# Optimization experiments

Hardware: AMD Instinct MI355X
Metric: run time of the kernel (lower is better)

Reference implementation:

```python
import jax, jax.numpy as jnp
import numpy as np

BLOCK_SIZE = 32
FP6_E2M3_MAX = 7.5

def _build_fp6_e2m3_grid():
    vals = set()
    for bits in range(64):
        s = (bits >> 5) & 1
        e = (bits >> 3) & 3
        m = bits & 7
        v = (m / 8.0) if e == 0 else (1.0 + m / 8.0) * 2.0 ** (e - 1)
        vals.add(-v if s else v)
    return np.array(sorted(vals), dtype=np.float32)

_GRID = jnp.asarray(_build_fp6_e2m3_grid())  # sorted 1-D fp32 grid (46 unique values)

def _nearest_on_grid(x, grid):
    # round-to-nearest on a sorted grid via searchsorted (matches torch reference)
    idx = jnp.clip(jnp.searchsorted(grid, x), 0, grid.shape[0] - 1)
    idx_lo = jnp.maximum(idx - 1, 0)
    v_hi = grid[idx]
    v_lo = grid[idx_lo]
    return jnp.where(jnp.abs(x - v_lo) <= jnp.abs(x - v_hi), v_lo, v_hi)

def _mx_quantize(t, eps=1e-30):
    # t: (rows, K) fp32, K divisible by BLOCK_SIZE
    rows, K = t.shape
    blocks = t.reshape(rows, K // BLOCK_SIZE, BLOCK_SIZE)
    scales = jnp.maximum(jnp.max(jnp.abs(blocks), axis=-1) / FP6_E2M3_MAX, eps)  # (rows, nb)
    q = _nearest_on_grid(blocks / scales[..., None], _GRID)  # fp6-simulated fp32
    return q, scales

def setup_inputs() -> dict:
    key = jax.random.key(0)
    k1, k2, k3 = jax.random.split(key, 3)
    x = jax.random.normal(k1, (8, 8192, 1024), dtype=jnp.float32)
    weight = jax.random.normal(k2, (1024, 1024), dtype=jnp.float32) * 0.02
    bias = jax.random.normal(k3, (1024,), dtype=jnp.float32) * 0.02
    return {"x": x, "weight": weight, "bias": bias}

def reference(x, weight, bias):
    batch_shape = x.shape[:-1]
    in_features = x.shape[-1]
    x2 = x.astype(jnp.float32).reshape(-1, in_features)      # (N, K)
    w2 = weight.astype(jnp.float32)                           # (J, K)
    xq, xs = _mx_quantize(x2)                                 # (N, nb, bs), (N, nb)
    wq, ws = _mx_quantize(w2)                                 # (J, nb, bs), (J, nb)
    # out[n, j] = sum_b xs[n,b] * ws[j,b] * dot(xq[n,b,:], wq[j,b,:])
    # == dequant(x) @ dequant(w).T  (fold fp32 scales into quantized blocks)
    xd = (xq * xs[..., None]).reshape(x2.shape)
    wd = (wq * ws[..., None]).reshape(w2.shape)
    out = xd @ wd.T + bias
    return out.reshape(*batch_shape, -1)
```

## Files before the change

kernel.cpp:

```cpp
#include <hip/hip_runtime.h>
#include <stdint.h>

#define K_DIM 1024
#define N_DIM 1024
#define M_DIM 65536

typedef __bf16 bf16_t;
typedef __bf16 bf16x8 __attribute__((ext_vector_type(8)));
typedef float f32x4 __attribute__((ext_vector_type(4)));

#define GLOAD_LDS16(g, l) __builtin_amdgcn_global_load_lds( \
    (const __attribute__((address_space(1))) void*)(g),     \
    (__attribute__((address_space(3))) void*)(l), 16, 0, 0)

#define VMCNT(n) asm volatile("s_waitcnt vmcnt(%0)" ::"n"(n) : "memory")
#define LGKM(n) asm volatile("s_waitcnt lgkmcnt(%0)" ::"n"(n) : "memory")
#define SCHEDB() __builtin_amdgcn_sched_barrier(0)

__global__ __launch_bounds__(256) void quant_dequant_kernel(
    const float* __restrict__ x, bf16_t* __restrict__ xd, long long nx,
    const float* __restrict__ w, bf16_t* __restrict__ wd, long long nw) {
  const float* in;
  bf16_t* out;
  long long i, stride, n;
  if (blockIdx.x < 512) {
    in = w; out = wd; n = nw;
    i = (long long)blockIdx.x * blockDim.x + threadIdx.x;
    stride = 512ll * blockDim.x;
  } else {
    in = x; out = xd; n = nx;
    i = (long long)(blockIdx.x - 512) * blockDim.x + threadIdx.x;
    stride = (long long)(gridDim.x - 512) * blockDim.x;
  }
  for (; i < n; i += stride) {
    long long base = i * 8;
    f32x4 v0 = *reinterpret_cast<const f32x4*>(in + base);
    f32x4 v1 = *reinterpret_cast<const f32x4*>(in + base + 4);
    float mx = 0.0f;
#pragma unroll
    for (int j = 0; j < 4; ++j) {
      mx = fmaxf(mx, fabsf(v0[j]));
      mx = fmaxf(mx, fabsf(v1[j]));
    }
    mx = fmaxf(mx, __shfl_xor(mx, 1));
    mx = fmaxf(mx, __shfl_xor(mx, 2));
    float s = fmaxf(mx / 7.5f, 1e-30f);
    bf16x8 o;
#pragma unroll
    for (int j = 0; j < 8; ++j) {
      float xv = (j < 4) ? v0[j] : v1[j - 4];
      float y = xv / s;
      float m = fabsf(y);
      float h, hinv;
      if (m < 2.0f)      { h = 0.125f; hinv = 8.0f; }
      else if (m < 4.0f) { h = 0.25f;  hinv = 4.0f; }
      else               { h = 0.5f;   hinv = 2.0f; }
      float nn = m * hinv;
      float kf = floorf(nn);
      float fr = nn - kf;
      float up = (fr > 0.5f || (fr == 0.5f && y < 0.0f)) ? 1.0f : 0.0f;
      float q = fminf((kf + up) * h, 7.5f);
      o[j] = (bf16_t)(copysignf(q, y) * s);
    }
    *reinterpret_cast<bf16x8*>(out + base) = o;
  }
}

__global__ __launch_bounds__(512, 2) void mx_gemm(
    const bf16_t* __restrict__ A, const bf16_t* __restrict__ B,
    const float* __restrict__ bias, float* __restrict__ C) {
  __shared__ char lds[131072];

  const int tid = threadIdx.x;
  const int lane = tid & 63;
  const int wid = tid >> 6;
  const int wm = wid >> 2;
  const int wn = wid & 3;

  const int b = blockIdx.x;
  const int xcd = b & 7;
  const int t = b >> 3;
  const int m_tile = xcd * 32 + (t >> 2);
  const int n_tile = t & 3;

  const int R0 = tid >> 2;
  const int c0 = ((tid & 3) ^ ((tid >> 3) & 3)) * 8;
  const bf16_t* aS0 = A + (size_t)(m_tile * 256 + R0) * K_DIM + c0;
  const bf16_t* aS1 = aS0 + (size_t)128 * K_DIM;
  const bf16_t* bS0 = B + (size_t)(n_tile * 256 + R0) * K_DIM + c0;
  const bf16_t* bS1 = bS0 + (size_t)128 * K_DIM;
  const int dstOff = tid * 16;

#define STAGE_A(u)                                  \
  {                                                 \
    char* sd_ = lds + ((u) & 3) * 32768;            \
    const int ko_ = (u) * 32;                       \
    GLOAD_LDS16(aS0 + ko_, sd_ + dstOff);           \
    GLOAD_LDS16(aS1 + ko_, sd_ + 8192 + dstOff);    \
  }
#define STAGE_B(u)                                  \
  {                                                 \
    char* sd_ = lds + ((u) & 3) * 32768;            \
    const int ko_ = (u) * 32;                       \
    GLOAD_LDS16(bS0 + ko_, sd_ + 16384 + dstOff);   \
    GLOAD_LDS16(bS1 + ko_, sd_ + 24576 + dstOff);   \
  }

  const int ps = (((lane >> 4) ^ ((lane >> 1) & 3)) << 4);
  const int rowb = (lane & 15) * 64 + ps;
  const int aOff = wm * 8192 + rowb;
  const int bOff = 16384 + wn * 4096 + rowb;

  f32x4 acc[8][4];
#pragma unroll
  for (int i = 0; i < 8; ++i)
#pragma unroll
    for (int j = 0; j < 4; ++j) acc[i][j] = (f32x4)(0.0f);

  bf16x8 bf[4], afA[4], afB[4];

#define PH_A(T, VMN, DO_STG)                                              \
  {                                                                       \
    const char* sb_ = lds + ((T) & 3) * 32768;                            \
    _Pragma("unroll") for (int j = 0; j < 4; ++j) bf[j] =                 \
        *reinterpret_cast<const bf16x8*>(sb_ + bOff + j * 1024);          \
    _Pragma("unroll") for (int i = 0; i < 4; ++i) afA[i] =                \
        *reinterpret_cast<const bf16x8*>(sb_ + aOff + i * 1024);          \
    if (DO_STG) STAGE_A((T) + 3);                                         \
    VMCNT(VMN);                                                           \
    __builtin_amdgcn_s_barrier();                                         \
    LGKM(0);                                                              \
    SCHEDB();                                                             \
    __builtin_amdgcn_s_setprio(1);                                        \
    _Pragma("unroll") for (int i = 0; i < 4; ++i)                         \
        _Pragma("unroll") for (int j = 0; j < 4; ++j) acc[i][j] =         \
            __builtin_amdgcn_mfma_f32_16x16x32_bf16(afA[i], bf[j],        \
                                                    acc[i][j], 0, 0, 0);  \
    __builtin_amdgcn_s_setprio(0);                                        \
    __builtin_amdgcn_s_barrier();                                         \
  }

#define PH_B(T, VMN, DO_STG)                                                 \
  {                                                                          \
    const char* sb_ = lds + ((T) & 3) * 32768;                               \
    _Pragma("unroll") for (int i = 0; i < 4; ++i) afB[i] =                   \
        *reinterpret_cast<const bf16x8*>(sb_ + aOff + 4096 + i * 1024);      \
    if (DO_STG) STAGE_B((T) + 3);                                            \
    VMCNT(VMN);                                                              \
    __builtin_amdgcn_s_barrier();                                            \
    LGKM(0);                                                                 \
    SCHEDB();                                                                \
    __builtin_amdgcn_s_setprio(1);                                           \
    _Pragma("unroll") for (int i = 0; i < 4; ++i)                            \
        _Pragma("unroll") for (int j = 0; j < 4; ++j) acc[4 + i][j] =        \
            __builtin_amdgcn_mfma_f32_16x16x32_bf16(afB[i], bf[j],           \
                                                    acc[4 + i][j], 0, 0, 0); \
    __builtin_amdgcn_s_setprio(0);                                           \
    __builtin_amdgcn_s_barrier();                                            \
  }

  STAGE_A(0); STAGE_B(0);
  STAGE_A(1); STAGE_B(1);
  STAGE_A(2); STAGE_B(2);
  VMCNT(8);
  __builtin_amdgcn_s_barrier();

  for (int kt = 0; kt < 29; ++kt) {
    PH_A(kt, 8, true);
    PH_B(kt, 8, true);
  }
  PH_A(29, 8, false);
  PH_B(29, 4, false);
  PH_A(30, 4, false);
  PH_B(30, 0, false);
  {
    const char* sb_ = lds + (31 & 3) * 32768;
#pragma unroll
    for (int j = 0; j < 4; ++j)
      bf[j] = *reinterpret_cast<const bf16x8*>(sb_ + bOff + j * 1024);
#pragma unroll
    for (int i = 0; i < 4; ++i)
      afA[i] = *reinterpret_cast<const bf16x8*>(sb_ + aOff + i * 1024);
#pragma unroll
    for (int i = 0; i < 4; ++i)
      afB[i] = *reinterpret_cast<const bf16x8*>(sb_ + aOff + 4096 + i * 1024);
    LGKM(0);
    SCHEDB();
#pragma unroll
    for (int i = 0; i < 4; ++i)
#pragma unroll
      for (int j = 0; j < 4; ++j) {
        acc[i][j] = __builtin_amdgcn_mfma_f32_16x16x32_bf16(afA[i], bf[j],
                                                            acc[i][j], 0, 0, 0);
        acc[4 + i][j] = __builtin_amdgcn_mfma_f32_16x16x32_bf16(
            afB[i], bf[j], acc[4 + i][j], 0, 0, 0);
      }
  }

  const int col0 = n_tile * 256 + wn * 64 + (lane & 15);
  const int row0 = m_tile * 256 + wm * 128 + ((lane >> 4) << 2);
#pragma unroll
  for (int j = 0; j < 4; ++j) {
    float bv = bias[col0 + j * 16];
#pragma unroll
    for (int m = 0; m < 8; ++m) {
#pragma unroll
      for (int r = 0; r < 4; ++r) {
        C[(size_t)(row0 + m * 16 + r) * N_DIM + col0 + j * 16] =
            acc[m][j][r] + bv;
      }
    }
  }
#undef STAGE_A
#undef STAGE_B
#undef PH_A
#undef PH_B
}

extern "C" void kernel_launch(void* const* d_in, const int* in_sizes, int n_in,
                              void* d_out, int out_size, void* d_ws,
                              size_t ws_size, hipStream_t stream) {
  const float* x = (const float*)d_in[0];
  const float* w = (const float*)d_in[1];
  const float* bias = (const float*)d_in[2];
  float* out = (float*)d_out;

  bf16_t* xd = (bf16_t*)d_ws;
  bf16_t* wd = xd + (size_t)M_DIM * K_DIM;

  quant_dequant_kernel<<<4608, 256, 0, stream>>>(
      x, xd, (long long)M_DIM * K_DIM / 8, w, wd,
      (long long)K_DIM * N_DIM / 8);

  mx_gemm<<<(M_DIM / 256) * (N_DIM / 256), 512, 0, stream>>>(xd, wd, bias,
                                                             out);
}
```

Baseline: 275.2 us.

## Load B fragments directly from global memory and restructure GEMM pipeline

The GEMM stops staging the B (weight) tile through LDS and has each wave read its B fragments directly from global memory into registers, double-buffered one k-step ahead. A is still staged into a smaller four-slot LDS ring, with register-level double buffering of A fragments and one barrier per k-step instead of two. The goal is to halve LDS use and traffic and cut barrier overhead. The cost is that B now comes from uncoalesced 16-byte global reads, which depend on L2 hits and put VMEM latency on the critical path. The VMCNT(0) wait at the start of every step also limits how far loads can run ahead.

```diff
diff --git a/kernel.cpp b/kernel.cpp
--- a/kernel.cpp
+++ b/kernel.cpp
@@ -69,7 +69,7 @@
 __global__ __launch_bounds__(512, 2) void mx_gemm(
     const bf16_t* __restrict__ A, const bf16_t* __restrict__ B,
     const float* __restrict__ bias, float* __restrict__ C) {
-  __shared__ char lds[131072];
+  __shared__ char lds[65536];
 
   const int tid = threadIdx.x;
   const int lane = tid & 63;
@@ -87,29 +87,17 @@
   const int c0 = ((tid & 3) ^ ((tid >> 3) & 3)) * 8;
   const bf16_t* aS0 = A + (size_t)(m_tile * 256 + R0) * K_DIM + c0;
   const bf16_t* aS1 = aS0 + (size_t)128 * K_DIM;
-  const bf16_t* bS0 = B + (size_t)(n_tile * 256 + R0) * K_DIM + c0;
-  const bf16_t* bS1 = bS0 + (size_t)128 * K_DIM;
-  const int dstOff = tid * 16;
-
-#define STAGE_A(u)                                  \
-  {                                                 \
-    char* sd_ = lds + ((u) & 3) * 32768;            \
-    const int ko_ = (u) * 32;                       \
-    GLOAD_LDS16(aS0 + ko_, sd_ + dstOff);           \
-    GLOAD_LDS16(aS1 + ko_, sd_ + 8192 + dstOff);    \
-  }
-#define STAGE_B(u)                                  \
-  {                                                 \
-    char* sd_ = lds + ((u) & 3) * 32768;            \
-    const int ko_ = (u) * 32;                       \
-    GLOAD_LDS16(bS0 + ko_, sd_ + 16384 + dstOff);   \
-    GLOAD_LDS16(bS1 + ko_, sd_ + 24576 + dstOff);   \
-  }
+  const int dst16 = tid * 16;
 
   const int ps = (((lane >> 4) ^ ((lane >> 1) & 3)) << 4);
-  const int rowb = (lane & 15) * 64 + ps;
-  const int aOff = wm * 8192 + rowb;
-  const int bOff = 16384 + wn * 4096 + rowb;
+  const int aRd = wm * 8192 + (lane & 15) * 64 + ps;
+
+  const char* Bb = (const char*)B;
+  int boffj[4];
+#pragma unroll
+  for (int j = 0; j < 4; ++j)
+    boffj[j] = (n_tile * 256 + wn * 64 + j * 16 + (lane & 15)) * 2048 +
+               (lane >> 4) * 16;
 
   f32x4 acc[8][4];
 #pragma unroll
@@ -117,85 +105,74 @@
 #pragma unroll
     for (int j = 0; j < 4; ++j) acc[i][j] = (f32x4)(0.0f);
 
-  bf16x8 bf[4], afA[4], afB[4];
-
-#define PH_A(T, VMN, DO_STG)                                              \
-  {                                                                       \
-    const char* sb_ = lds + ((T) & 3) * 32768;                            \
-    _Pragma("unroll") for (int j = 0; j < 4; ++j) bf[j] =                 \
-        *reinterpret_cast<const bf16x8*>(sb_ + bOff + j * 1024);          \
-    _Pragma("unroll") for (int i = 0; i < 4; ++i) afA[i] =                \
-        *reinterpret_cast<const bf16x8*>(sb_ + aOff + i * 1024);          \
-    if (DO_STG) STAGE_A((T) + 3);                                         \
-    VMCNT(VMN);                                                           \
-    __builtin_amdgcn_s_barrier();                                         \
-    LGKM(0);                                                              \
-    SCHEDB();                                                             \
-    __builtin_amdgcn_s_setprio(1);                                        \
-    _Pragma("unroll") for (int i = 0; i < 4; ++i)                         \
-        _Pragma("unroll") for (int j = 0; j < 4; ++j) acc[i][j] =         \
-            __builtin_amdgcn_mfma_f32_16x16x32_bf16(afA[i], bf[j],        \
-                                                    acc[i][j], 0, 0, 0);  \
-    __builtin_amdgcn_s_setprio(0);                                        \
-    __builtin_amdgcn_s_barrier();                                         \
-  }
-
-#define PH_B(T, VMN, DO_STG)                                                 \
-  {                                                                          \
-    const char* sb_ = lds + ((T) & 3) * 32768;                               \
-    _Pragma("unroll") for (int i = 0; i < 4; ++i) afB[i] =                   \
-        *reinterpret_cast<const bf16x8*>(sb_ + aOff + 4096 + i * 1024);      \
-    if (DO_STG) STAGE_B((T) + 3);                                            \
-    VMCNT(VMN);                                                              \
-    __builtin_amdgcn_s_barrier();                                            \
-    LGKM(0);                                                                 \
-    SCHEDB();                                                                \
-    __builtin_amdgcn_s_setprio(1);                                           \
-    _Pragma("unroll") for (int i = 0; i < 4; ++i)                            \
-        _Pragma("unroll") for (int j = 0; j < 4; ++j) acc[4 + i][j] =        \
-            __builtin_amdgcn_mfma_f32_16x16x32_bf16(afB[i], bf[j],           \
-                                                    acc[4 + i][j], 0, 0, 0); \
-    __builtin_amdgcn_s_setprio(0);                                           \
-    __builtin_amdgcn_s_barrier();                                            \
-  }
-
-  STAGE_A(0); STAGE_B(0);
-  STAGE_A(1); STAGE_B(1);
-  STAGE_A(2); STAGE_B(2);
-  VMCNT(8);
+  bf16x8 a[2][8], bfr[2][4];
+
+#define BODY(Q, PAR, STG, DOB, DOA, LG)                                       \
+  {                                                                           \
+    VMCNT(0);                                                                 \
+    __builtin_amdgcn_s_barrier();                                             \
+    SCHEDB();                                                                 \
+    if (STG) {                                                                \
+      GLOAD_LDS16(aS0 + ((Q) + 2) * 32,                                       \
+                  lds + (((Q) + 2) & 3) * 16384 + dst16);                     \
+      GLOAD_LDS16(aS1 + ((Q) + 2) * 32,                                       \
+                  lds + (((Q) + 2) & 3) * 16384 + 8192 + dst16);              \
+    }                                                                         \
+    if (DOB) {                                                                \
+      _Pragma("unroll") for (int j = 0; j < 4; ++j)                           \
+          bfr[(PAR) ^ 1][j] = *reinterpret_cast<const bf16x8*>(               \
+              Bb + boffj[j] + ((Q) + 1) * 64);                                \
+    }                                                                         \
+    if (DOA) {                                                                \
+      const char* sb_ = lds + (((Q) + 1) & 3) * 16384;                        \
+      _Pragma("unroll") for (int i = 0; i < 4; ++i) {                         \
+        a[(PAR) ^ 1][i] =                                                     \
+            *reinterpret_cast<const bf16x8*>(sb_ + aRd + i * 1024);           \
+        a[(PAR) ^ 1][4 + i] =                                                 \
+            *reinterpret_cast<const bf16x8*>(sb_ + aRd + 4096 + i * 1024);    \
+      }                                                                       \
+    }                                                                         \
+    SCHEDB();                                                                 \
+    LGKM(LG);                                                                 \
+    SCHEDB();                                                                 \
+    __builtin_amdgcn_s_setprio(1);                                            \
+    _Pragma("unroll") for (int i = 0; i < 8; ++i)                             \
+        _Pragma("unroll") for (int j = 0; j < 4; ++j) acc[i][j] =             \
+            __builtin_amdgcn_mfma_f32_16x16x32_bf16(a[PAR][i], bfr[PAR][j],   \
+                                                    acc[i][j], 0, 0, 0);      \
+    __builtin_amdgcn_s_setprio(0);                                            \
+  }
+
+  GLOAD_LDS16(aS0, lds + dst16);
+  GLOAD_LDS16(aS1, lds + 8192 + dst16);
+  GLOAD_LDS16(aS0 + 32, lds + 16384 + dst16);
+  GLOAD_LDS16(aS1 + 32, lds + 16384 + 8192 + dst16);
+#pragma unroll
+  for (int j = 0; j < 4; ++j)
+    bfr[0][j] = *reinterpret_cast<const bf16x8*>(Bb + boffj[j]);
+  VMCNT(4);
   __builtin_amdgcn_s_barrier();
-
-  for (int kt = 0; kt < 29; ++kt) {
-    PH_A(kt, 8, true);
-    PH_B(kt, 8, true);
-  }
-  PH_A(29, 8, false);
-  PH_B(29, 4, false);
-  PH_A(30, 4, false);
-  PH_B(30, 0, false);
-  {
-    const char* sb_ = lds + (31 & 3) * 32768;
-#pragma unroll
-    for (int j = 0; j < 4; ++j)
-      bf[j] = *reinterpret_cast<const bf16x8*>(sb_ + bOff + j * 1024);
-#pragma unroll
-    for (int i = 0; i < 4; ++i)
-      afA[i] = *reinterpret_cast<const bf16x8*>(sb_ + aOff + i * 1024);
-#pragma unroll
-    for (int i = 0; i < 4; ++i)
-      afB[i] = *reinterpret_cast<const bf16x8*>(sb_ + aOff + 4096 + i * 1024);
-    LGKM(0);
-    SCHEDB();
-#pragma unroll
-    for (int i = 0; i < 4; ++i)
-#pragma unroll
-      for (int j = 0; j < 4; ++j) {
-        acc[i][j] = __builtin_amdgcn_mfma_f32_16x16x32_bf16(afA[i], bf[j],
-                                                            acc[i][j], 0, 0, 0);
-        acc[4 + i][j] = __builtin_amdgcn_mfma_f32_16x16x32_bf16(
-            afB[i], bf[j], acc[4 + i][j], 0, 0, 0);
-      }
-  }
+  SCHEDB();
+#pragma unroll
+  for (int i = 0; i < 4; ++i) {
+    a[0][i] = *reinterpret_cast<const bf16x8*>(lds + aRd + i * 1024);
+    a[0][4 + i] = *reinterpret_cast<const bf16x8*>(lds + aRd + 4096 + i * 1024);
+  }
+
+  for (int p = 0; p < 7; ++p) {
+    BODY(0, 0, 1, 1, 1, 8);
+    BODY(1, 1, 1, 1, 1, 8);
+    BODY(2, 0, 1, 1, 1, 8);
+    BODY(3, 1, 1, 1, 1, 8);
+    aS0 += 128;
+    aS1 += 128;
+#pragma unroll
+    for (int j = 0; j < 4; ++j) boffj[j] += 256;
+  }
+  BODY(0, 0, 1, 1, 1, 8);
+  BODY(1, 1, 1, 1, 1, 8);
+  BODY(2, 0, 0, 1, 1, 8);
+  BODY(3, 1, 0, 0, 0, 0);
 
   const int col0 = n_tile * 256 + wn * 64 + (lane & 15);
   const int row0 = m_tile * 256 + wm * 128 + ((lane >> 4) << 2);
@@ -211,10 +188,7 @@
       }
     }
   }
-#undef STAGE_A
-#undef STAGE_B
-#undef PH_A
-#undef PH_B
+#undef BODY
 }
 
 extern "C" void kernel_launch(void* const* d_in, const int* in_sizes, int n_in,
```

Result: slower. 368.7 us (+34.0%).
